# Kernel optimization log

Measured on AMD Instinct MI355X. Metric: run time of the kernel, lower is better.

The kernel has to match this reference:

```python
import jax, jax.numpy as jnp
import numpy as np

N_NODES = 50000
N_EDGES = 800000
D = 64


def setup_inputs() -> dict:
    key = jax.random.key(0)
    k = jax.random.split(key, 8)
    h = jax.random.normal(k[0], (N_NODES, D), dtype=jnp.float32)
    edge_src = jax.random.randint(k[1], (N_EDGES,), 0, N_NODES, dtype=jnp.int32)
    edge_dst = jax.random.randint(k[2], (N_EDGES,), 0, N_NODES, dtype=jnp.int32)
    # normalized adjacency weights (e.g. 1/deg style values in (0,1))
    edge_w = jax.random.uniform(k[3], (N_EDGES,), dtype=jnp.float32)
    W_self = jax.random.normal(k[4], (D, D), dtype=jnp.float32) / np.sqrt(D)
    b_self = jnp.zeros((D,), dtype=jnp.float32)
    W_neigh = jax.random.normal(k[5], (D, D), dtype=jnp.float32) / np.sqrt(D)
    b_neigh = jnp.zeros((D,), dtype=jnp.float32)
    return {
        "h": h,
        "edge_src": edge_src,
        "edge_dst": edge_dst,
        "edge_w": edge_w,
        "W_self": W_self,
        "b_self": b_self,
        "W_neigh": W_neigh,
        "b_neigh": b_neigh,
    }


def reference(h, edge_src, edge_dst, edge_w, W_self, b_self, W_neigh, b_neigh):
    # neigh = A_norm @ h : sparse COO matmul as weighted gather + segment-sum
    # messages: [E, D]
    msgs = edge_w[:, None] * h[edge_src]
    neigh = jax.ops.segment_sum(msgs, edge_dst, num_segments=N_NODES)  # [N, D]
    # out = lin_self(h) + lin_neigh(neigh), relu; dropout is a no-op in eval mode
    out = (h @ W_self.T + b_self) + (neigh @ W_neigh.T + b_neigh)
    return jax.nn.relu(out)
```

## Files before the change

kernel.cpp:

```cpp
#include <hip/hip_runtime.h>

#define N_NODES 50000
#define N_EDGES 800000
#define D 64

#define NPB 200
#define NB  250
#define CAP 4096
#define BT  512
#define EPT 8
#define CHUNK_E (BT * EPT)
#define NCHUNKS ((N_EDGES + CHUNK_E - 1) / CHUNK_E)
#define CONVB 256
#define CT  1024
#define NTILE ((NPB + 15) / 16)

typedef unsigned short ushort_t;
typedef unsigned int   uint_t;
typedef __attribute__((ext_vector_type(8))) short   short8;
typedef __attribute__((ext_vector_type(4))) float   float4v;

__device__ __forceinline__ ushort_t f2b(float f) {
    uint_t u = __float_as_uint(f);
    return (ushort_t)((u + 0x7FFFu + ((u >> 16) & 1u)) >> 16);
}
__device__ __forceinline__ float b2f(ushort_t b) {
    return __uint_as_float((uint_t)b << 16);
}
__device__ __forceinline__ uint_t rne_hi16(uint_t u) {
    return (u + 0x7FFFu + ((u >> 16) & 1u)) & 0xFFFF0000u;
}
__device__ __forceinline__ float lane_bcast(float v, int l) {
    return __int_as_float(__builtin_amdgcn_readlane(__float_as_int(v), l));
}


__global__ __launch_bounds__(BT) void bin_h2b_kernel(
    const int* __restrict__ src, const int* __restrict__ dst,
    const float* __restrict__ w, int* __restrict__ cursor,
    int2* __restrict__ bedges,
    const float* __restrict__ h, ushort_t* __restrict__ hb)
{
    if (blockIdx.x >= NCHUNKS) {
        const int nb = gridDim.x - NCHUNKS;
        for (int i = (blockIdx.x - NCHUNKS) * BT + threadIdx.x;
             i < N_NODES * D / 4; i += nb * BT) {
            const float4 v = ((const float4*)h)[i];
            ushort4 o;
            o.x = f2b(v.x); o.y = f2b(v.y); o.z = f2b(v.z); o.w = f2b(v.w);
            ((ushort4*)hb)[i] = o;
        }
        return;
    }

    __shared__ int lh[NB];
    __shared__ int loff[NB];
    __shared__ int lcur[NB];
    __shared__ int gpos[NB];
    __shared__ int part[256];
    __shared__ int2 stage[CHUNK_E];
    __shared__ unsigned char sbk[CHUNK_E];

    const int t = threadIdx.x;
    for (int i = t; i < NB; i += BT) lh[i] = 0;
    __syncthreads();

    const int base = blockIdx.x * CHUNK_E;
    int   my_b[EPT];
    int   my_p[EPT];
    float my_w[EPT];
#pragma unroll
    for (int k = 0; k < EPT; ++k) {
        const int e = base + k * BT + t;
        if (e < N_EDGES) {
            const int d = dst[e];
            const int b = (unsigned)d / NPB;
            my_b[k] = b;
            my_p[k] = (src[e] << 8) | (d - b * NPB);
            my_w[k] = w[e];
            atomicAdd(&lh[b], 1);
        } else {
            my_b[k] = -1;
        }
    }
    __syncthreads();

    const int v = (t < NB) ? lh[t] : 0;
    if (t < 256) part[t] = v;
    __syncthreads();
    for (int off = 1; off < 256; off <<= 1) {
        int p = 0;
        if (t < 256 && t >= off) p = part[t - off];
        __syncthreads();
        if (t < 256) part[t] += p;
        __syncthreads();
    }
    if (t < NB) { loff[t] = part[t] - v; lcur[t] = part[t] - v; }
    __syncthreads();

#pragma unroll
    for (int k = 0; k < EPT; ++k) {
        if (my_b[k] >= 0) {
            const int p = atomicAdd(&lcur[my_b[k]], 1);
            stage[p] = make_int2(my_p[k], __float_as_int(my_w[k]));
            sbk[p] = (unsigned char)my_b[k];
        }
    }
    __syncthreads();

    if (t < NB && lh[t] > 0)
        gpos[t] = t * CAP + atomicAdd(&cursor[t], lh[t]);
    __syncthreads();

    const int tot = min(N_EDGES - base, CHUNK_E);
    for (int s = t; s < tot; s += BT) {
        const int b = sbk[s];
        bedges[gpos[b] + (s - loff[b])] = stage[s];
    }
}

__global__ __launch_bounds__(CT) void csr_gather_kernel(
    const int* __restrict__ cursor, const int2* __restrict__ bedges,
    const ushort_t* __restrict__ hb,
    const float* __restrict__ Ws, const float* __restrict__ bs,
    const float* __restrict__ Wn, const float* __restrict__ bn,
    float* __restrict__ out)
{
    __shared__ int      offs[NPB + 1];
    __shared__ int      lcur[NPB];
    __shared__ int      part[256];
    __shared__ __align__(16) uint_t   stage[CAP];
    __shared__ __align__(16) ushort_t nstage[NTILE * 16 * D];

    const int b   = blockIdx.x;
    const int t   = threadIdx.x;
    const int gb  = b * CAP;
    const int cnt = min(cursor[b], CAP);

    if (t < NPB) lcur[t] = 0;
    __syncthreads();
    for (int e = t; e < cnt; e += CT)
        atomicAdd(&lcur[bedges[gb + e].x & 255], 1);
    __syncthreads();

    const int v = (t < NPB) ? lcur[t] : 0;
    if (t < 256) part[t] = v;
    __syncthreads();
    for (int off = 1; off < 256; off <<= 1) {
        int p = 0;
        if (t < 256 && t >= off) p = part[t - off];
        __syncthreads();
        if (t < 256) part[t] += p;
        __syncthreads();
    }
    if (t < NPB) {
        const int ex = part[t] - v;
        offs[t] = ex;
        lcur[t] = ex;
    }
    if (t == 0) offs[NPB] = cnt;
    if (t < (NTILE * 16 - NPB) * D) nstage[NPB * D + t] = 0;
    __syncthreads();

    for (int e = t; e < cnt; e += CT) {
        const int2 r = bedges[gb + e];
        const int p = atomicAdd(&lcur[r.x & 255], 1);
        stage[p] = (uint_t)(r.x >> 8) | rne_hi16((uint_t)r.y);
    }
    __syncthreads();

    const int wave = t >> 6;
    const int lane = t & 63;
    const int nbeg = wave * 12 + min(wave, 8);
    const int ncnt = 12 + (wave < 8 ? 1 : 0);
    for (int ni = 0; ni < ncnt; ++ni) {
        const int n   = nbeg + ni;
        const int beg = offs[n], end = offs[n + 1];
        float acc = 0.f;
        int e = beg;
        for (; e + 8 <= end; e += 8) {
            uint_t r[8];
            float  vv[8];
#pragma unroll
            for (int k = 0; k < 8; ++k) r[k] = stage[e + k];
#pragma unroll
            for (int k = 0; k < 8; ++k)
                vv[k] = b2f(hb[(size_t)(r[k] & 0xFFFFu) * D + lane]);
#pragma unroll
            for (int k = 0; k < 8; ++k)
                acc = fmaf(__uint_as_float(r[k] & 0xFFFF0000u), vv[k], acc);
        }
        for (; e < end; ++e) {
            const uint_t r = stage[e];
            acc = fmaf(__uint_as_float(r & 0xFFFF0000u),
                       b2f(hb[(size_t)(r & 0xFFFFu) * D + lane]), acc);
        }
        nstage[n * D + lane] = f2b(acc);
    }
    __syncthreads();

    const int node0b = b * NPB;
    const int row16  = lane & 15;
    const int quad   = lane >> 4;
    for (int task = wave; task < NTILE * 4; task += 16) {
        const int m  = task >> 2;
        const int nt = task & 3;
        const int arow = m * 16 + row16;

        const size_t abase = (size_t)(node0b + arow) * D + quad * 8;
        const short8 ah0 = *(const short8*)(hb + abase);
        const short8 ah1 = *(const short8*)(hb + abase + 32);
        const ushort_t* sp = nstage + arow * D + quad * 8;
        const short8 an0 = *(const short8*)sp;
        const short8 an1 = *(const short8*)(sp + 32);

        const int col = nt * 16 + row16;
        const float* wsr = Ws + (size_t)col * D + quad * 8;
        const float* wnr = Wn + (size_t)col * D + quad * 8;
        short8 bw[4];
#pragma unroll
        for (int f = 0; f < 4; ++f) {
            const float* p = (f < 2 ? wsr : wnr) + (f & 1) * 32;
            const float4 w0 = *(const float4*)p;
            const float4 w1 = *(const float4*)(p + 4);
            short8 bwv;
            bwv[0] = (short)f2b(w0.x); bwv[1] = (short)f2b(w0.y);
            bwv[2] = (short)f2b(w0.z); bwv[3] = (short)f2b(w0.w);
            bwv[4] = (short)f2b(w1.x); bwv[5] = (short)f2b(w1.y);
            bwv[6] = (short)f2b(w1.z); bwv[7] = (short)f2b(w1.w);
            bw[f] = bwv;
        }
        float4v acc = {0.f, 0.f, 0.f, 0.f};
        acc = __builtin_amdgcn_mfma_f32_16x16x32_bf16(ah0, bw[0], acc, 0, 0, 0);
        acc = __builtin_amdgcn_mfma_f32_16x16x32_bf16(ah1, bw[1], acc, 0, 0, 0);
        acc = __builtin_amdgcn_mfma_f32_16x16x32_bf16(an0, bw[2], acc, 0, 0, 0);
        acc = __builtin_amdgcn_mfma_f32_16x16x32_bf16(an1, bw[3], acc, 0, 0, 0);

        const float bias = bs[col] + bn[col];
#pragma unroll
        for (int r = 0; r < 4; ++r) {
            const int mr = m * 16 + quad * 4 + r;
            if (mr < NPB)
                out[(size_t)(node0b + mr) * D + col] = fmaxf(acc[r] + bias, 0.f);
        }
    }
}

__global__ __launch_bounds__(256) void sage_scatter(
    const float* __restrict__ h,
    const int* __restrict__ edge_src,
    const int* __restrict__ edge_dst,
    const float* __restrict__ edge_w,
    float* __restrict__ neigh)
{
    const long long tid = (long long)blockIdx.x * blockDim.x + threadIdx.x;
    const int e = (int)(tid >> 6);
    const int d = (int)(tid & 63);
    if (e >= N_EDGES) return;
    atomicAdd(&neigh[(long long)edge_dst[e] * D + d],
              edge_w[e] * h[(long long)edge_src[e] * D + d]);
}

__global__ __launch_bounds__(256, 2) void linear_f32_kernel(
    const float* __restrict__ h, const float* __restrict__ neigh,
    const float* __restrict__ Ws, const float* __restrict__ bs,
    const float* __restrict__ Wn, const float* __restrict__ bn,
    float* __restrict__ out)
{
    const int lane   = threadIdx.x & 63;
    const int gwave  = (blockIdx.x * blockDim.x + threadIdx.x) >> 6;
    const int nwaves = (gridDim.x * blockDim.x) >> 6;

    float Wsr[D], Wnr[D];
#pragma unroll
    for (int k = 0; k < D; k += 4) {
        const float4 a = *(const float4*)&Ws[(size_t)lane * D + k];
        const float4 b = *(const float4*)&Wn[(size_t)lane * D + k];
        Wsr[k] = a.x; Wsr[k+1] = a.y; Wsr[k+2] = a.z; Wsr[k+3] = a.w;
        Wnr[k] = b.x; Wnr[k+1] = b.y; Wnr[k+2] = b.z; Wnr[k+3] = b.w;
    }
    const float bias = bs[lane] + bn[lane];

    for (int n = gwave; n < N_NODES; n += nwaves) {
        const float hv = h[(size_t)n * D + lane];
        const float nv = neigh[(size_t)n * D + lane];
        float o = bias;
#pragma unroll
        for (int k = 0; k < D; ++k) {
            o = fmaf(lane_bcast(hv, k), Wsr[k], o);
            o = fmaf(lane_bcast(nv, k), Wnr[k], o);
        }
        out[(size_t)n * D + lane] = fmaxf(o, 0.f);
    }
}

extern "C" void kernel_launch(void* const* d_in, const int* in_sizes, int n_in,
                              void* d_out, int out_size, void* d_ws, size_t ws_size,
                              hipStream_t stream)
{
    const float* h        = (const float*)d_in[0];
    const int*   edge_src = (const int*)d_in[1];
    const int*   edge_dst = (const int*)d_in[2];
    const float* edge_w   = (const float*)d_in[3];
    const float* W_self   = (const float*)d_in[4];
    const float* b_self   = (const float*)d_in[5];
    const float* W_neigh  = (const float*)d_in[6];
    const float* b_neigh  = (const float*)d_in[7];
    float*       out      = (float*)d_out;

    int2*     bedges = (int2*)d_ws;
    ushort_t* hb     = (ushort_t*)(bedges + (size_t)NB * CAP);
    int*      cursor = (int*)(hb + (size_t)N_NODES * D);
    const size_t needed = (size_t)NB * CAP * 8 + (size_t)N_NODES * D * 2 + NB * 4;

    if (ws_size >= needed) {
        hipMemsetAsync(cursor, 0, NB * sizeof(int), stream);
        bin_h2b_kernel<<<NCHUNKS + CONVB, BT, 0, stream>>>(
            edge_src, edge_dst, edge_w, cursor, bedges, h, hb);
        csr_gather_kernel<<<NB, CT, 0, stream>>>(
            cursor, bedges, hb, W_self, b_self, W_neigh, b_neigh, out);
    } else {
        float* neigh_fb = (float*)d_ws;
        hipMemsetAsync(neigh_fb, 0, (size_t)N_NODES * D * sizeof(float), stream);
        const long long total = (long long)N_EDGES * 64;
        sage_scatter<<<(int)((total + 255) / 256), 256, 0, stream>>>(
            h, edge_src, edge_dst, edge_w, neigh_fb);
        linear_f32_kernel<<<1024, 256, 0, stream>>>(h, neigh_fb, W_self, b_self,
                                                    W_neigh, b_neigh, out);
    }
}
```

Baseline: 142.2 us.

## Split each destination bucket across two half-size gather blocks

The gather kernel now launches two 512-thread blocks per 200-node bucket instead of one 1024-thread block, and each block handles 100 destination nodes. Both blocks scan the full bucket edge list and keep only edges whose local node index falls in their half. This is meant to raise the block count and improve occupancy and load balance, since 250 blocks underfill the GPU. The cost is that every bucket's edge list is read twice, and a half-sized stage buffer has to clamp writes in case a half overflows.

Result: no change. 143.4 us (+0.8%).

```diff
diff --git a/kernel.cpp b/kernel.cpp
--- a/kernel.cpp
+++ b/kernel.cpp
@@ -12,8 +12,11 @@
 #define CHUNK_E (BT * EPT)
 #define NCHUNKS ((N_EDGES + CHUNK_E - 1) / CHUNK_E)
 #define CONVB 256
-#define CT  1024
-#define NTILE ((NPB + 15) / 16)
+
+#define CGT 512
+#define NPH 100
+#define HCAP 2048
+#define NTILE ((NPH + 15) / 16)
 
 typedef unsigned short ushort_t;
 typedef unsigned int   uint_t;
@@ -119,63 +122,71 @@
     }
 }
 
-__global__ __launch_bounds__(CT) void csr_gather_kernel(
+__global__ __launch_bounds__(CGT) void csr_gather_kernel(
     const int* __restrict__ cursor, const int2* __restrict__ bedges,
     const ushort_t* __restrict__ hb,
     const float* __restrict__ Ws, const float* __restrict__ bs,
     const float* __restrict__ Wn, const float* __restrict__ bn,
     float* __restrict__ out)
 {
-    __shared__ int      offs[NPB + 1];
-    __shared__ int      lcur[NPB];
-    __shared__ int      part[256];
-    __shared__ __align__(16) uint_t   stage[CAP];
+    __shared__ int      offs[NPH + 1];
+    __shared__ int      lcur[NPH];
+    __shared__ int      part[128];
+    __shared__ __align__(16) uint_t   stage[HCAP];
     __shared__ __align__(16) ushort_t nstage[NTILE * 16 * D];
 
-    const int b   = blockIdx.x;
+    const int blk = blockIdx.x;
+    const int b   = blk >> 1;
+    const int lo  = (blk & 1) * NPH;
     const int t   = threadIdx.x;
     const int gb  = b * CAP;
     const int cnt = min(cursor[b], CAP);
 
-    if (t < NPB) lcur[t] = 0;
-    __syncthreads();
-    for (int e = t; e < cnt; e += CT)
-        atomicAdd(&lcur[bedges[gb + e].x & 255], 1);
-    __syncthreads();
-
-    const int v = (t < NPB) ? lcur[t] : 0;
-    if (t < 256) part[t] = v;
-    __syncthreads();
-    for (int off = 1; off < 256; off <<= 1) {
+    if (t < NPH) lcur[t] = 0;
+    __syncthreads();
+    for (int e = t; e < cnt; e += CGT) {
+        const unsigned ll = (unsigned)((bedges[gb + e].x & 255) - lo);
+        if (ll < NPH) atomicAdd(&lcur[ll], 1);
+    }
+    __syncthreads();
+
+    const int v = (t < NPH) ? lcur[t] : 0;
+    if (t < 128) part[t] = v;
+    __syncthreads();
+    for (int off = 1; off < 128; off <<= 1) {
         int p = 0;
-        if (t < 256 && t >= off) p = part[t - off];
+        if (t < 128 && t >= off) p = part[t - off];
         __syncthreads();
-        if (t < 256) part[t] += p;
+        if (t < 128) part[t] += p;
         __syncthreads();
     }
-    if (t < NPB) {
+    if (t < NPH) {
         const int ex = part[t] - v;
         offs[t] = ex;
         lcur[t] = ex;
     }
-    if (t == 0) offs[NPB] = cnt;
-    if (t < (NTILE * 16 - NPB) * D) nstage[NPB * D + t] = 0;
-    __syncthreads();
-
-    for (int e = t; e < cnt; e += CT) {
+    if (t == 0) offs[NPH] = part[127];
+    for (int i = t; i < (NTILE * 16 - NPH) * D; i += CGT) nstage[NPH * D + i] = 0;
+    __syncthreads();
+
+    for (int e = t; e < cnt; e += CGT) {
         const int2 r = bedges[gb + e];
-        const int p = atomicAdd(&lcur[r.x & 255], 1);
-        stage[p] = (uint_t)(r.x >> 8) | rne_hi16((uint_t)r.y);
+        const unsigned ll = (unsigned)((r.x & 255) - lo);
+        if (ll < NPH) {
+            const int p = atomicAdd(&lcur[ll], 1);
+            stage[min(p, HCAP - 1)] = (uint_t)(r.x >> 8) | rne_hi16((uint_t)r.y);
+        }
     }
     __syncthreads();
 
     const int wave = t >> 6;
     const int lane = t & 63;
-    const int nbeg = wave * 12 + min(wave, 8);
-    const int ncnt = 12 + (wave < 8 ? 1 : 0);
+    const int nbeg = wave * 12 + min(wave, 4);
+    const int ncnt = 12 + (wave < 4 ? 1 : 0);
     for (int ni = 0; ni < ncnt; ++ni) {
         const int n   = nbeg + ni;
-        const int beg = offs[n], end = offs[n + 1];
+        const int beg = min(offs[n], HCAP);
+        const int end = min(offs[n + 1], HCAP);
         float acc = 0.f;
         int e = beg;
         for (; e + 8 <= end; e += 8) {
@@ -199,15 +210,15 @@
     }
     __syncthreads();
 
-    const int node0b = b * NPB;
+    const int node0  = b * NPB + lo;
     const int row16  = lane & 15;
     const int quad   = lane >> 4;
-    for (int task = wave; task < NTILE * 4; task += 16) {
+    for (int task = wave; task < NTILE * 4; task += 8) {
         const int m  = task >> 2;
         const int nt = task & 3;
         const int arow = m * 16 + row16;
 
-        const size_t abase = (size_t)(node0b + arow) * D + quad * 8;
+        const size_t abase = (size_t)(node0 + arow) * D + quad * 8;
         const short8 ah0 = *(const short8*)(hb + abase);
         const short8 ah1 = *(const short8*)(hb + abase + 32);
         const ushort_t* sp = nstage + arow * D + quad * 8;
@@ -240,8 +251,8 @@
 #pragma unroll
         for (int r = 0; r < 4; ++r) {
             const int mr = m * 16 + quad * 4 + r;
-            if (mr < NPB)
-                out[(size_t)(node0b + mr) * D + col] = fmaxf(acc[r] + bias, 0.f);
+            if (mr < NPH)
+                out[(size_t)(node0 + mr) * D + col] = fmaxf(acc[r] + bias, 0.f);
         }
     }
 }
@@ -317,7 +328,7 @@
         hipMemsetAsync(cursor, 0, NB * sizeof(int), stream);
         bin_h2b_kernel<<<NCHUNKS + CONVB, BT, 0, stream>>>(
             edge_src, edge_dst, edge_w, cursor, bedges, h, hb);
-        csr_gather_kernel<<<NB, CT, 0, stream>>>(
+        csr_gather_kernel<<<NB * 2, CGT, 0, stream>>>(
             cursor, bedges, hb, W_self, b_self, W_neigh, b_neigh, out);
     } else {
         float* neigh_fb = (float*)d_ws;
```
